# Kernel optimization log

Hardware: AMD Instinct MI355X
Metric: run time of the kernel (lower is better)

Reference implementation:

```python
import jax, jax.numpy as jnp
import numpy as np
from jax import lax

N_HEADS = 16
TOP_K = 2
N_EXPERTS = 8

def layer_norm(x, w, b, eps=1e-5):
    mu = jnp.mean(x, axis=-1, keepdims=True)
    var = jnp.mean(jnp.square(x - mu), axis=-1, keepdims=True)
    return (x - mu) * lax.rsqrt(var + eps) * w + b

def attention(x, w_qkv, b_qkv, w_o, b_o):
    B, T, D = x.shape
    dh = D // N_HEADS
    qkv = x @ w_qkv + b_qkv                       # [B,T,3D]
    q, k, v = jnp.split(qkv, 3, axis=-1)
    q = q.reshape(B, T, N_HEADS, dh)
    k = k.reshape(B, T, N_HEADS, dh)
    v = v.reshape(B, T, N_HEADS, dh)
    scores = jnp.einsum('bqhd,bkhd->bhqk', q, k) / jnp.sqrt(jnp.float32(dh)).astype(x.dtype)
    probs = jax.nn.softmax(scores, axis=-1)
    ctx = jnp.einsum('bhqk,bkhd->bqhd', probs, v).reshape(B, T, D)
    return ctx @ w_o + b_o

def moe_ff(x, w_gate, w1, b1, w2, b2):
    # top-k token routing (dropless: equivalent math to gate_and_sort ->
    # dispatch -> grouped expert GEMM -> combine -> unpermute)
    B, T, D = x.shape
    t = x.reshape(B * T, D)                        # [N,D]
    probs = jax.nn.softmax(t @ w_gate, axis=-1)    # [N,E]
    tw, ti = lax.top_k(probs, TOP_K)               # [N,K]
    tw = tw / jnp.sum(tw, axis=-1, keepdims=True)  # renormalize top-k weights
    out = jnp.zeros_like(t)
    for e in range(N_EXPERTS):
        we = jnp.sum(jnp.where(ti == e, tw, 0.0), axis=-1)       # [N]
        h = jax.nn.gelu(t @ w1[e] + b1[e]) @ w2[e] + b2[e]       # expert FFN
        out = out + we[:, None] * h
    return out.reshape(B, T, D)

def reference(x, ln1_w, ln1_b, ln2_w, ln2_b, w_qkv, b_qkv, w_o, b_o, w_gate, w1, b1, w2, b2):
    # pre-norm transformer block: attention then MoE FFN, both residual.
    # The torch module's 2-way micro-batch pipelining is per-token identical
    # to full-batch compute, so we compute the full batch at once.
    h = x + attention(layer_norm(x, ln1_w, ln1_b), w_qkv, b_qkv, w_o, b_o)
    return h + moe_ff(layer_norm(h, ln2_w, ln2_b), w_gate, w1, b1, w2, b2)

def setup_inputs() -> dict:
    key = jax.random.key(0)
    ks = jax.random.split(key, 8)
    B, T, D, H, E = 4, 512, 1024, 4096, 8
    s = lambda d: 1.0 / np.sqrt(d)
    return {
        'x': jax.random.normal(ks[0], (B, T, D), jnp.float32),
        'ln1_w': jnp.ones((D,), jnp.float32),
        'ln1_b': jnp.zeros((D,), jnp.float32),
        'ln2_w': jnp.ones((D,), jnp.float32),
        'ln2_b': jnp.zeros((D,), jnp.float32),
        'w_qkv': jax.random.normal(ks[1], (D, 3 * D), jnp.float32) * s(D),
        'b_qkv': jnp.zeros((3 * D,), jnp.float32),
        'w_o': jax.random.normal(ks[2], (D, D), jnp.float32) * s(D),
        'b_o': jnp.zeros((D,), jnp.float32),
        'w_gate': jax.random.normal(ks[3], (D, E), jnp.float32) * s(D),
        'w1': jax.random.normal(ks[4], (E, D, H), jnp.float32) * s(D),
        'b1': jnp.zeros((E, H), jnp.float32),
        'w2': jax.random.normal(ks[5], (E, H, D), jnp.float32) * s(H),
        'b2': jnp.zeros((E, D), jnp.float32),
    }
```

## Files before the change

### kernel.cpp

```cpp
#include <hip/hip_runtime.h>
#include <math.h>

typedef unsigned short ushort_t;
using short8 = __attribute__((ext_vector_type(8))) short;
using f32x4  = __attribute__((ext_vector_type(4))) float;

#define N_TOK 2048
#define DIM   1024
#define D3    3072
#define NHEAD 16
#define DH    64
#define TT    512
#define HID   4096
#define NEXP  8

__device__ __forceinline__ float bf2f(ushort_t u){
  union { unsigned int i; float f; } x; x.i = ((unsigned int)u) << 16; return x.f;
}
__device__ __forceinline__ ushort_t f2bf(float f){
  union { unsigned int i; float f; } x; x.f = f;
  unsigned int r = x.i + 0x7fffu + ((x.i >> 16) & 1u);
  return (ushort_t)(r >> 16);
}
__device__ __forceinline__ float gelu_f(float x){
  const float c = 0.7978845608028654f;
  float t = tanhf(c * (x + 0.044715f * x * x * x));
  return 0.5f * x * (1.0f + t);
}

template<int MODE>
__global__ __launch_bounds__(256) void ln_k(const float* __restrict__ xin,
                                            const float* __restrict__ w,
                                            const float* __restrict__ b,
                                            float* __restrict__ out,
                                            ushort_t* __restrict__ outhi,
                                            ushort_t* __restrict__ outlo){
  int tok = blockIdx.x;
  int t = threadIdx.x;
  float vals[4]; float s = 0.f, ss = 0.f;
#pragma unroll
  for (int i = 0; i < 4; i++){
    int d = t + i * 256;
    float v = xin[(size_t)tok * DIM + d];
    vals[i] = v; s += v; ss += v * v;
  }
  __shared__ float rs[256], rq[256];
  rs[t] = s; rq[t] = ss; __syncthreads();
  for (int k = 128; k > 0; k >>= 1){
    if (t < k){ rs[t] += rs[t + k]; rq[t] += rq[t + k]; }
    __syncthreads();
  }
  float mu  = rs[0] * (1.0f / DIM);
  float var = rq[0] * (1.0f / DIM) - mu * mu;
  float inv = rsqrtf(var + 1e-5f);
#pragma unroll
  for (int i = 0; i < 4; i++){
    int d = t + i * 256;
    float r = (vals[i] - mu) * inv * w[d] + b[d];
    size_t idx = (size_t)tok * DIM + d;
    if (MODE == 1){
      out[idx] = r;
      outhi[idx] = f2bf(r);
    } else {
      ushort_t hv = f2bf(r);
      outhi[idx] = hv;
      outlo[idx] = f2bf(r - bf2f(hv));
    }
  }
}

__global__ __launch_bounds__(256) void convT2(const float* __restrict__ src,
                                              ushort_t* __restrict__ dhi,
                                              ushort_t* __restrict__ dlo,
                                              int R, int C){
  __shared__ float tile[64][65];
  int r0 = blockIdx.y * 64, c0 = blockIdx.x * 64;
  int t = threadIdx.x;
  int tc = t & 15, tr = t >> 4;
#pragma unroll
  for (int i = 0; i < 4; i++){
    int r = tr + i * 16;
    float4 v = *(const float4*)&src[(size_t)(r0 + r) * C + c0 + tc * 4];
    tile[r][tc*4 + 0] = v.x; tile[r][tc*4 + 1] = v.y;
    tile[r][tc*4 + 2] = v.z; tile[r][tc*4 + 3] = v.w;
  }
  __syncthreads();
#pragma unroll
  for (int i = 0; i < 4; i++){
    int c = tr + i * 16;
    float v0 = tile[tc*4 + 0][c];
    float v1 = tile[tc*4 + 1][c];
    float v2 = tile[tc*4 + 2][c];
    float v3 = tile[tc*4 + 3][c];
    ushort4 oh, ol;
    oh.x = f2bf(v0); ol.x = f2bf(v0 - bf2f(oh.x));
    oh.y = f2bf(v1); ol.y = f2bf(v1 - bf2f(oh.y));
    oh.z = f2bf(v2); ol.z = f2bf(v2 - bf2f(oh.z));
    oh.w = f2bf(v3); ol.w = f2bf(v3 - bf2f(oh.w));
    size_t o = (size_t)(c0 + c) * R + r0 + tc * 4;
    *(ushort4*)&dhi[o] = oh;
    *(ushort4*)&dlo[o] = ol;
  }
}

__global__ __launch_bounds__(256) void convT_g(const float* __restrict__ src0,
                                               ushort_t* __restrict__ dst0,
                                               int R, int C){
  size_t eo = (size_t)blockIdx.z * R * C;
  const float* src = src0 + eo;
  ushort_t* dst = dst0 + eo;
  __shared__ float tile[64][65];
  int r0 = blockIdx.y * 64, c0 = blockIdx.x * 64;
  int t = threadIdx.x;
  int tc = t & 15, tr = t >> 4;
#pragma unroll
  for (int i = 0; i < 4; i++){
    int r = tr + i * 16;
    float4 v = *(const float4*)&src[(size_t)(r0 + r) * C + c0 + tc * 4];
    tile[r][tc*4 + 0] = v.x; tile[r][tc*4 + 1] = v.y;
    tile[r][tc*4 + 2] = v.z; tile[r][tc*4 + 3] = v.w;
  }
  __syncthreads();
#pragma unroll
  for (int i = 0; i < 4; i++){
    int c = tr + i * 16;
    ushort4 o;
    o.x = f2bf(tile[tc*4 + 0][c]);
    o.y = f2bf(tile[tc*4 + 1][c]);
    o.z = f2bf(tile[tc*4 + 2][c]);
    o.w = f2bf(tile[tc*4 + 3][c]);
    *(ushort4*)&dst[(size_t)(c0 + c) * R + r0 + tc * 4] = o;
  }
}

#define TBM 128
#define TBN 128
#define TBK 32
#define LDK 40

template<int EPI>
__global__ __launch_bounds__(256) void gemm_split(
    const ushort_t* __restrict__ Ahi, const ushort_t* __restrict__ Alo,
    const ushort_t* __restrict__ Bhi, const ushort_t* __restrict__ Blo,
    const float* __restrict__ bias,
    float* __restrict__ C, const float* __restrict__ Res,
    int Nn, int K)
{
  int bm = blockIdx.y * TBM, bn = blockIdx.x * TBN;
  __shared__ ushort_t Ah[TBM * LDK];
  __shared__ ushort_t Al[TBM * LDK];
  __shared__ ushort_t Bh[TBN * LDK];
  __shared__ ushort_t Bl[TBN * LDK];
  int t = threadIdx.x;
  int lane = t & 63, wave = t >> 6;
  int wm = (wave & 1) * 64, wn = (wave >> 1) * 64;

  int r0 = t >> 2, r1 = r0 + 64;
  int kc = (t & 3) * 8;
  const ushort_t* ah0 = Ahi + (size_t)(bm + r0) * K + kc;
  const ushort_t* ah1 = Ahi + (size_t)(bm + r1) * K + kc;
  const ushort_t* al0 = Alo + (size_t)(bm + r0) * K + kc;
  const ushort_t* al1 = Alo + (size_t)(bm + r1) * K + kc;
  const ushort_t* bh0 = Bhi + (size_t)(bn + r0) * K + kc;
  const ushort_t* bh1 = Bhi + (size_t)(bn + r1) * K + kc;
  const ushort_t* bl0 = Blo + (size_t)(bn + r0) * K + kc;
  const ushort_t* bl1 = Blo + (size_t)(bn + r1) * K + kc;

  f32x4 acc[4][4] = {};
  int fm = lane & 15, fk = (lane >> 4) * 8;

  for (int k0 = 0; k0 < K; k0 += TBK){
    uint4 vah0 = *(const uint4*)(ah0 + k0);
    uint4 vah1 = *(const uint4*)(ah1 + k0);
    uint4 val0 = *(const uint4*)(al0 + k0);
    uint4 val1 = *(const uint4*)(al1 + k0);
    uint4 vbh0 = *(const uint4*)(bh0 + k0);
    uint4 vbh1 = *(const uint4*)(bh1 + k0);
    uint4 vbl0 = *(const uint4*)(bl0 + k0);
    uint4 vbl1 = *(const uint4*)(bl1 + k0);
    *(uint4*)&Ah[r0 * LDK + kc] = vah0;
    *(uint4*)&Ah[r1 * LDK + kc] = vah1;
    *(uint4*)&Al[r0 * LDK + kc] = val0;
    *(uint4*)&Al[r1 * LDK + kc] = val1;
    *(uint4*)&Bh[r0 * LDK + kc] = vbh0;
    *(uint4*)&Bh[r1 * LDK + kc] = vbh1;
    *(uint4*)&Bl[r0 * LDK + kc] = vbl0;
    *(uint4*)&Bl[r1 * LDK + kc] = vbl1;
    __syncthreads();
    short8 afh[4], afl[4], bfh[4], bfl[4];
#pragma unroll
    for (int mi = 0; mi < 4; mi++){
      afh[mi] = *(const short8*)&Ah[(wm + mi*16 + fm) * LDK + fk];
      afl[mi] = *(const short8*)&Al[(wm + mi*16 + fm) * LDK + fk];
    }
#pragma unroll
    for (int nj = 0; nj < 4; nj++){
      bfh[nj] = *(const short8*)&Bh[(wn + nj*16 + fm) * LDK + fk];
      bfl[nj] = *(const short8*)&Bl[(wn + nj*16 + fm) * LDK + fk];
    }
#pragma unroll
    for (int mi = 0; mi < 4; mi++)
#pragma unroll
      for (int nj = 0; nj < 4; nj++){
        acc[mi][nj] = __builtin_amdgcn_mfma_f32_16x16x32_bf16(afh[mi], bfh[nj], acc[mi][nj], 0, 0, 0);
        acc[mi][nj] = __builtin_amdgcn_mfma_f32_16x16x32_bf16(afh[mi], bfl[nj], acc[mi][nj], 0, 0, 0);
        acc[mi][nj] = __builtin_amdgcn_mfma_f32_16x16x32_bf16(afl[mi], bfh[nj], acc[mi][nj], 0, 0, 0);
      }
    __syncthreads();
  }

#pragma unroll
  for (int mi = 0; mi < 4; mi++){
    int rowbase = bm + wm + mi*16 + (lane >> 4) * 4;
#pragma unroll
    for (int nj = 0; nj < 4; nj++){
      int n = bn + wn + nj*16 + (lane & 15);
      f32x4 v = acc[mi][nj];
#pragma unroll
      for (int rg = 0; rg < 4; rg++){
        size_t idx = (size_t)(rowbase + rg) * Nn + n;
        float val = v[rg] + bias[n];
        if (EPI == 1) val += Res[idx];
        C[idx] = val;
      }
    }
  }
}

__global__ __launch_bounds__(256) void scores_k(const float* __restrict__ qkv,
                                                float* __restrict__ S){
  int bh = blockIdx.z; int b = bh >> 4, h = bh & 15;
  int q0 = blockIdx.y * 64, k0 = blockIdx.x * 64;
  __shared__ float Qs[64][68];
  __shared__ float Ks[64][68];
  int t = threadIdx.x;
  int r = t >> 2, dp = (t & 3) * 16;
  {
    const float* qp = qkv + (size_t)(b * TT + q0 + r) * D3 + h * DH + dp;
    const float* kp = qkv + (size_t)(b * TT + k0 + r) * D3 + DIM + h * DH + dp;
#pragma unroll
    for (int c = 0; c < 4; c++){
      float4 qv = *(const float4*)(qp + c * 4);
      float4 kv = *(const float4*)(kp + c * 4);
      Qs[dp + c*4 + 0][r] = qv.x; Qs[dp + c*4 + 1][r] = qv.y;
      Qs[dp + c*4 + 2][r] = qv.z; Qs[dp + c*4 + 3][r] = qv.w;
      Ks[dp + c*4 + 0][r] = kv.x; Ks[dp + c*4 + 1][r] = kv.y;
      Ks[dp + c*4 + 2][r] = kv.z; Ks[dp + c*4 + 3][r] = kv.w;
    }
  }
  __syncthreads();
  int tx = t & 15, ty = t >> 4;
  float acc[4][4] = {};
#pragma unroll 8
  for (int d = 0; d < 64; d++){
    float4 qv = *(const float4*)&Qs[d][ty * 4];
    float4 kv = *(const float4*)&Ks[d][tx * 4];
    float qa[4] = {qv.x,qv.y,qv.z,qv.w};
    float ka[4] = {kv.x,kv.y,kv.z,kv.w};
#pragma unroll
    for (int i = 0; i < 4; i++)
#pragma unroll
      for (int j = 0; j < 4; j++)
        acc[i][j] += qa[i] * ka[j];
  }
#pragma unroll
  for (int i = 0; i < 4; i++)
#pragma unroll
    for (int j = 0; j < 4; j++)
      S[((size_t)bh * TT + q0 + ty*4 + i) * TT + k0 + tx*4 + j] = acc[i][j] * 0.125f;
}

__global__ __launch_bounds__(256) void softmax_k(float* __restrict__ S){
  size_t row = blockIdx.x;
  float* p = S + row * TT;
  int t = threadIdx.x;
  float v0 = p[t], v1 = p[t + 256];
  __shared__ float red[256];
  red[t] = fmaxf(v0, v1); __syncthreads();
  for (int k = 128; k > 0; k >>= 1){ if (t < k) red[t] = fmaxf(red[t], red[t + k]); __syncthreads(); }
  float m = red[0]; __syncthreads();
  float e0 = expf(v0 - m), e1 = expf(v1 - m);
  red[t] = e0 + e1; __syncthreads();
  for (int k = 128; k > 0; k >>= 1){ if (t < k) red[t] += red[t + k]; __syncthreads(); }
  float inv = 1.0f / red[0];
  p[t] = e0 * inv; p[t + 256] = e1 * inv;
}

__global__ __launch_bounds__(256) void ctx_k(const float* __restrict__ P,
                                             const float* __restrict__ qkv,
                                             ushort_t* __restrict__ chi,
                                             ushort_t* __restrict__ clo){
  int bh = blockIdx.y; int b = bh >> 4, h = bh & 15;
  int q0 = blockIdx.x * 64;
  __shared__ float Ps[16][68];
  __shared__ float Vs[16][68];
  int t = threadIdx.x;
  int tx = t & 15, ty = t >> 4;
  int pq = t >> 2, pk = (t & 3) * 4;
  int vk = t >> 4, vd = (t & 15) * 4;
  float acc[4][4] = {};
  for (int kk = 0; kk < TT; kk += 16){
    float4 pv = *(const float4*)&P[((size_t)bh * TT + q0 + pq) * TT + kk + pk];
    Ps[pk + 0][pq] = pv.x; Ps[pk + 1][pq] = pv.y;
    Ps[pk + 2][pq] = pv.z; Ps[pk + 3][pq] = pv.w;
    float4 vv = *(const float4*)&qkv[(size_t)(b * TT + kk + vk) * D3 + 2 * DIM + h * DH + vd];
    Vs[vk][vd + 0] = vv.x; Vs[vk][vd + 1] = vv.y;
    Vs[vk][vd + 2] = vv.z; Vs[vk][vd + 3] = vv.w;
    __syncthreads();
#pragma unroll
    for (int k = 0; k < 16; k++){
      float4 a = *(const float4*)&Ps[k][ty * 4];
      float4 bb = *(const float4*)&Vs[k][tx * 4];
      float aa[4] = {a.x,a.y,a.z,a.w};
      float bv[4] = {bb.x,bb.y,bb.z,bb.w};
#pragma unroll
      for (int i = 0; i < 4; i++)
#pragma unroll
        for (int j = 0; j < 4; j++)
          acc[i][j] += aa[i] * bv[j];
    }
    __syncthreads();
  }
#pragma unroll
  for (int i = 0; i < 4; i++)
#pragma unroll
    for (int j = 0; j < 4; j++){
      float v = acc[i][j];
      size_t idx = (size_t)(b * TT + q0 + ty*4 + i) * DIM + h * DH + tx*4 + j;
      ushort_t hv = f2bf(v);
      chi[idx] = hv;
      clo[idx] = f2bf(v - bf2f(hv));
    }
}

__global__ __launch_bounds__(256) void gate_k(const float* __restrict__ ln2f,
                                              const float* __restrict__ wg,
                                              float* __restrict__ we){
  int tok = blockIdx.x * 4 + (threadIdx.x >> 6);
  int lane = threadIdx.x & 63;
  float acc[8] = {};
  for (int d = lane; d < DIM; d += 64){
    float x = ln2f[(size_t)tok * DIM + d];
    float4 w0 = *(const float4*)&wg[d * 8];
    float4 w1v = *(const float4*)&wg[d * 8 + 4];
    float wv[8] = {w0.x,w0.y,w0.z,w0.w,w1v.x,w1v.y,w1v.z,w1v.w};
#pragma unroll
    for (int e = 0; e < 8; e++) acc[e] += x * wv[e];
  }
#pragma unroll
  for (int off = 32; off > 0; off >>= 1){
#pragma unroll
    for (int e = 0; e < 8; e++) acc[e] += __shfl_down(acc[e], off);
  }
  if (lane == 0){
    float m = acc[0];
    for (int e = 1; e < 8; e++) m = fmaxf(m, acc[e]);
    float pr[8], s = 0.f;
    for (int e = 0; e < 8; e++){ pr[e] = expf(acc[e] - m); s += pr[e]; }
    for (int e = 0; e < 8; e++) pr[e] /= s;
    int i0 = 0;
    for (int e = 1; e < 8; e++) if (pr[e] > pr[i0]) i0 = e;
    int i1 = (i0 == 0) ? 1 : 0;
    for (int e = 0; e < 8; e++) if (e != i0 && pr[e] > pr[i1]) i1 = e;
    float sm = pr[i0] + pr[i1];
    for (int e = 0; e < 8; e++)
      we[(size_t)tok * 8 + e] = (e == i0) ? pr[i0] / sm : ((e == i1) ? pr[i1] / sm : 0.f);
  }
}

__global__ __launch_bounds__(256) void route_k(const float* __restrict__ we,
                                               int* __restrict__ cnt,
                                               int* __restrict__ gidx,
                                               float* __restrict__ gw){
  int tok = blockIdx.x * 256 + threadIdx.x;
#pragma unroll
  for (int e = 0; e < NEXP; e++){
    float w = we[(size_t)tok * NEXP + e];
    if (w > 0.f){
      int p = atomicAdd(&cnt[e], 1);
      gidx[e * N_TOK + p] = tok;
      gw[e * N_TOK + p] = w;
    }
  }
}

__global__ void scan_k(const int* __restrict__ cnt, int* __restrict__ off){
  if (threadIdx.x == 0){
    int s = 0;
    for (int e = 0; e < NEXP; e++){ off[e] = s; s += cnt[e]; }
  }
}

template<int EPI>
__global__ __launch_bounds__(256) void moe_gemm_g(
    const ushort_t* __restrict__ A,
    const ushort_t* __restrict__ BT_all,
    const float* __restrict__ bias_all,
    ushort_t* __restrict__ Obf,
    float* __restrict__ Of,
    const int* __restrict__ gidx_all,
    const float* __restrict__ gw_all,
    const int* __restrict__ cnt,
    const int* __restrict__ off,
    int Nn, int K)
{
  int e  = blockIdx.y >> 4;
  int c  = cnt[e];
  int bm = (blockIdx.y & 15) * TBM;
  if (bm >= c) return;
  int bn = blockIdx.x * TBN;
  const int* gidx = gidx_all + e * N_TOK;
  const float* gwp = gw_all + e * N_TOK;
  const ushort_t* BT = BT_all + (size_t)e * Nn * K;
  const float* bias = bias_all + (size_t)e * Nn;
  int obase = off[e];

  __shared__ ushort_t As[TBM * LDK];
  __shared__ ushort_t Bs[TBN * LDK];
  int t = threadIdx.x;
  int lane = t & 63, wave = t >> 6;
  int wm = (wave & 1) * 64, wn = (wave >> 1) * 64;

  int r0 = t >> 2, r1 = r0 + 64;
  int kc = (t & 3) * 8;
  size_t ga0, ga1;
  if (EPI == 0){
    int g0 = bm + r0, g1 = bm + r1;
    ga0 = (size_t)((g0 < c) ? gidx[g0] : gidx[bm]);
    ga1 = (size_t)((g1 < c) ? gidx[g1] : gidx[bm]);
  } else {
    int mx = 2 * N_TOK - 1;
    int g0 = obase + bm + r0; if (g0 > mx) g0 = mx;
    int g1 = obase + bm + r1; if (g1 > mx) g1 = mx;
    ga0 = (size_t)g0; ga1 = (size_t)g1;
  }
  const ushort_t* a0p = A + ga0 * K + kc;
  const ushort_t* a1p = A + ga1 * K + kc;
  const ushort_t* b0p = BT + (size_t)(bn + r0) * K + kc;
  const ushort_t* b1p = BT + (size_t)(bn + r1) * K + kc;

  f32x4 acc[4][4] = {};
  int fm = lane & 15, fk = (lane >> 4) * 8;

  uint4 av0 = *(const uint4*)(a0p);
  uint4 av1 = *(const uint4*)(a1p);
  uint4 bv0 = *(const uint4*)(b0p);
  uint4 bv1 = *(const uint4*)(b1p);

  for (int k0 = 0; k0 < K; k0 += TBK){
    *(uint4*)&As[r0 * LDK + kc] = av0;
    *(uint4*)&As[r1 * LDK + kc] = av1;
    *(uint4*)&Bs[r0 * LDK + kc] = bv0;
    *(uint4*)&Bs[r1 * LDK + kc] = bv1;
    __syncthreads();
    int kn = k0 + TBK;
    if (kn < K){
      av0 = *(const uint4*)(a0p + kn);
      av1 = *(const uint4*)(a1p + kn);
      bv0 = *(const uint4*)(b0p + kn);
      bv1 = *(const uint4*)(b1p + kn);
    }
    short8 af[4], bfr[4];
#pragma unroll
    for (int mi = 0; mi < 4; mi++)
      af[mi] = *(const short8*)&As[(wm + mi*16 + fm) * LDK + fk];
#pragma unroll
    for (int nj = 0; nj < 4; nj++)
      bfr[nj] = *(const short8*)&Bs[(wn + nj*16 + fm) * LDK + fk];
#pragma unroll
    for (int mi = 0; mi < 4; mi++)
#pragma unroll
      for (int nj = 0; nj < 4; nj++)
        acc[mi][nj] = __builtin_amdgcn_mfma_f32_16x16x32_bf16(af[mi], bfr[nj], acc[mi][nj], 0, 0, 0);
    __syncthreads();
  }

#pragma unroll
  for (int mi = 0; mi < 4; mi++){
    int rowbase = bm + wm + mi*16 + (lane >> 4) * 4;
#pragma unroll
    for (int nj = 0; nj < 4; nj++){
      int n = bn + wn + nj*16 + (lane & 15);
      f32x4 v = acc[mi][nj];
#pragma unroll
      for (int rg = 0; rg < 4; rg++){
        int r = rowbase + rg;
        if (r < c){
          float val = v[rg] + bias[n];
          if (EPI == 0){
            Obf[(size_t)(obase + r) * Nn + n] = f2bf(gelu_f(val));
          } else {
            int tok = gidx[r];
            atomicAdd(&Of[(size_t)tok * Nn + n], gwp[r] * val);
          }
        }
      }
    }
  }
}

__global__ __launch_bounds__(256) void final_k(const float* __restrict__ h,
                                               const float* __restrict__ acc,
                                               float* __restrict__ out){
  size_t i = (size_t)blockIdx.x * 256 + threadIdx.x;
  out[i] = h[i] + acc[i];
}

extern "C" void kernel_launch(void* const* d_in, const int* in_sizes, int n_in,
                              void* d_out, int out_size, void* d_ws, size_t ws_size,
                              hipStream_t stream){
  const float* x     = (const float*)d_in[0];
  const float* ln1w  = (const float*)d_in[1];
  const float* ln1b  = (const float*)d_in[2];
  const float* ln2w  = (const float*)d_in[3];
  const float* ln2b  = (const float*)d_in[4];
  const float* wqkv  = (const float*)d_in[5];
  const float* bqkv  = (const float*)d_in[6];
  const float* wo    = (const float*)d_in[7];
  const float* bo    = (const float*)d_in[8];
  const float* wgate = (const float*)d_in[9];
  const float* w1    = (const float*)d_in[10];
  const float* b1    = (const float*)d_in[11];
  const float* w2    = (const float*)d_in[12];
  const float* b2    = (const float*)d_in[13];

  char* ws = (char*)d_ws;
  const size_t MB = 1024 * 1024;
  float*    hbuf  = (float*)(ws + 0 * MB);
  ushort_t* ln1hi = (ushort_t*)(ws + 0 * MB);
  ushort_t* ln1lo = (ushort_t*)(ws + 4 * MB);
  float*    accb  = (float*)(ws + 8 * MB);
  ushort_t* wqkvThi = (ushort_t*)(ws + 8 * MB);
  ushort_t* wqkvTlo = (ushort_t*)(ws + 14 * MB);
  ushort_t* ln2bf = (ushort_t*)(ws + 16 * MB);
  ushort_t* h1e   = (ushort_t*)(ws + 20 * MB);
  float*    qkv   = (float*)(ws + 20 * MB);
  float*    ln2f  = (float*)(ws + 24 * MB);
  ushort_t* ctxhi = (ushort_t*)(ws + 44 * MB);
  ushort_t* ctxlo = (ushort_t*)(ws + 48 * MB);
  ushort_t* woThi = (ushort_t*)(ws + 52 * MB);
  ushort_t* woTlo = (ushort_t*)(ws + 54 * MB);
  float*    sc    = (float*)(ws + 56 * MB);
  ushort_t* wTe   = (ushort_t*)(ws + 56 * MB);
  float*    webuf = (float*)(ws + 120 * MB);
  int*      cnt   = (int*)  (ws + 120 * MB + 256 * 1024);
  int*      off   = (int*)  (ws + 120 * MB + 260 * 1024);
  int*      bidx  = (int*)  (ws + 120 * MB + 320 * 1024);
  float*    bw    = (float*)(ws + 120 * MB + 448 * 1024);

  ln_k<2><<<N_TOK, 256, 0, stream>>>(x, ln1w, ln1b, nullptr, ln1hi, ln1lo);
  convT2<<<dim3(D3 / 64, DIM / 64), 256, 0, stream>>>(wqkv, wqkvThi, wqkvTlo, DIM, D3);
  gemm_split<0><<<dim3(D3 / TBN, N_TOK / TBM), 256, 0, stream>>>(
      ln1hi, ln1lo, wqkvThi, wqkvTlo, bqkv, qkv, nullptr, D3, DIM);
  scores_k<<<dim3(8, 8, 64), 256, 0, stream>>>(qkv, sc);
  softmax_k<<<64 * TT, 256, 0, stream>>>(sc);
  ctx_k<<<dim3(8, 64), 256, 0, stream>>>(sc, qkv, ctxhi, ctxlo);
  convT_g<<<dim3(HID / 64, DIM / 64, NEXP), 256, 0, stream>>>(w1, wTe, DIM, HID);
  convT2<<<dim3(DIM / 64, DIM / 64), 256, 0, stream>>>(wo, woThi, woTlo, DIM, DIM);
  gemm_split<1><<<dim3(DIM / TBN, N_TOK / TBM), 256, 0, stream>>>(
      ctxhi, ctxlo, woThi, woTlo, bo, hbuf, x, DIM, DIM);
  ln_k<1><<<N_TOK, 256, 0, stream>>>(hbuf, ln2w, ln2b, ln2f, ln2bf, nullptr);
  gate_k<<<N_TOK / 4, 256, 0, stream>>>(ln2f, wgate, webuf);

  hipMemsetAsync(cnt, 0, 32, stream);
  hipMemsetAsync(accb, 0, (size_t)N_TOK * DIM * 4, stream);
  route_k<<<N_TOK / 256, 256, 0, stream>>>(webuf, cnt, bidx, bw);
  scan_k<<<1, 64, 0, stream>>>(cnt, off);
  moe_gemm_g<0><<<dim3(HID / TBN, NEXP * 16), 256, 0, stream>>>(
      ln2bf, wTe, b1, h1e, nullptr, bidx, bw, cnt, off, HID, DIM);
  convT_g<<<dim3(DIM / 64, HID / 64, NEXP), 256, 0, stream>>>(w2, wTe, HID, DIM);
  moe_gemm_g<1><<<dim3(DIM / TBN, NEXP * 16), 256, 0, stream>>>(
      h1e, wTe, b2, nullptr, accb, bidx, bw, cnt, off, DIM, HID);
  final_k<<<(N_TOK * DIM) / 256, 256, 0, stream>>>(hbuf, accb, (float*)d_out);
}
```

Before: 772.9 us.

## Split-K the second MoE GEMM, remap block indices, prefetch in split GEMM

The second expert GEMM (K=4096) is split into four K-chunks of 1024, multiplying its block count. The chunks combine through the existing atomicAdd epilogue, with bias added only by the first chunk. The MoE kernels now use a 1D grid that interleaves experts across consecutive block IDs, and their K loop is unrolled by two with double register prefetch. The split-precision GEMMs get a remapped block order meant to help L2 locality/XCD spread, plus register prefetch of the next K tile. The cost is four times more atomic traffic into the accumulator and more register pressure.

```diff
diff --git a/kernel.cpp b/kernel.cpp
--- a/kernel.cpp
+++ b/kernel.cpp
@@ -144,9 +144,12 @@
     const ushort_t* __restrict__ Bhi, const ushort_t* __restrict__ Blo,
     const float* __restrict__ bias,
     float* __restrict__ C, const float* __restrict__ Res,
-    int Nn, int K)
+    int Nn, int K, int mblocks)
 {
-  int bm = blockIdx.y * TBM, bn = blockIdx.x * TBN;
+  int q = gridDim.x >> 3;
+  int L = (blockIdx.x & 7) * q + (blockIdx.x >> 3);
+  int bm = (L % mblocks) * TBM;
+  int bn = (L / mblocks) * TBN;
   __shared__ ushort_t Ah[TBM * LDK];
   __shared__ ushort_t Al[TBM * LDK];
   __shared__ ushort_t Bh[TBN * LDK];
@@ -169,15 +172,16 @@
   f32x4 acc[4][4] = {};
   int fm = lane & 15, fk = (lane >> 4) * 8;
 
+  uint4 vah0 = *(const uint4*)(ah0);
+  uint4 vah1 = *(const uint4*)(ah1);
+  uint4 val0 = *(const uint4*)(al0);
+  uint4 val1 = *(const uint4*)(al1);
+  uint4 vbh0 = *(const uint4*)(bh0);
+  uint4 vbh1 = *(const uint4*)(bh1);
+  uint4 vbl0 = *(const uint4*)(bl0);
+  uint4 vbl1 = *(const uint4*)(bl1);
+
   for (int k0 = 0; k0 < K; k0 += TBK){
-    uint4 vah0 = *(const uint4*)(ah0 + k0);
-    uint4 vah1 = *(const uint4*)(ah1 + k0);
-    uint4 val0 = *(const uint4*)(al0 + k0);
-    uint4 val1 = *(const uint4*)(al1 + k0);
-    uint4 vbh0 = *(const uint4*)(bh0 + k0);
-    uint4 vbh1 = *(const uint4*)(bh1 + k0);
-    uint4 vbl0 = *(const uint4*)(bl0 + k0);
-    uint4 vbl1 = *(const uint4*)(bl1 + k0);
     *(uint4*)&Ah[r0 * LDK + kc] = vah0;
     *(uint4*)&Ah[r1 * LDK + kc] = vah1;
     *(uint4*)&Al[r0 * LDK + kc] = val0;
@@ -187,6 +191,17 @@
     *(uint4*)&Bl[r0 * LDK + kc] = vbl0;
     *(uint4*)&Bl[r1 * LDK + kc] = vbl1;
     __syncthreads();
+    int kn = k0 + TBK;
+    if (kn < K){
+      vah0 = *(const uint4*)(ah0 + kn);
+      vah1 = *(const uint4*)(ah1 + kn);
+      val0 = *(const uint4*)(al0 + kn);
+      val1 = *(const uint4*)(al1 + kn);
+      vbh0 = *(const uint4*)(bh0 + kn);
+      vbh1 = *(const uint4*)(bh1 + kn);
+      vbl0 = *(const uint4*)(bl0 + kn);
+      vbl1 = *(const uint4*)(bl1 + kn);
+    }
     short8 afh[4], afl[4], bfh[4], bfl[4];
 #pragma unroll
     for (int mi = 0; mi < 4; mi++){
@@ -402,13 +417,20 @@
     const float* __restrict__ gw_all,
     const int* __restrict__ cnt,
     const int* __restrict__ off,
-    int Nn, int K)
+    int Nn)
 {
-  int e  = blockIdx.y >> 4;
-  int c  = cnt[e];
-  int bm = (blockIdx.y & 15) * TBM;
+  int rid = blockIdx.x;
+  int e = rid & 7;
+  int s = rid >> 3;
+  int c = cnt[e];
+  int bm = (s & 15) * TBM;
   if (bm >= c) return;
-  int bn = blockIdx.x * TBN;
+  int col, ks;
+  if (EPI == 0){ col = s >> 4; ks = 0; }
+  else         { col = (s >> 4) & 7; ks = s >> 7; }
+  const int K = (EPI == 0) ? DIM : HID;
+  int kbase = ks * 1024;
+  int bn = col * TBN;
   const int* gidx = gidx_all + e * N_TOK;
   const float* gwp = gw_all + e * N_TOK;
   const ushort_t* BT = BT_all + (size_t)e * Nn * K;
@@ -434,44 +456,78 @@
     int g1 = obase + bm + r1; if (g1 > mx) g1 = mx;
     ga0 = (size_t)g0; ga1 = (size_t)g1;
   }
-  const ushort_t* a0p = A + ga0 * K + kc;
-  const ushort_t* a1p = A + ga1 * K + kc;
-  const ushort_t* b0p = BT + (size_t)(bn + r0) * K + kc;
-  const ushort_t* b1p = BT + (size_t)(bn + r1) * K + kc;
+  const ushort_t* a0p = A + ga0 * K + kbase + kc;
+  const ushort_t* a1p = A + ga1 * K + kbase + kc;
+  const ushort_t* b0p = BT + (size_t)(bn + r0) * K + kbase + kc;
+  const ushort_t* b1p = BT + (size_t)(bn + r1) * K + kbase + kc;
 
   f32x4 acc[4][4] = {};
   int fm = lane & 15, fk = (lane >> 4) * 8;
 
-  uint4 av0 = *(const uint4*)(a0p);
-  uint4 av1 = *(const uint4*)(a1p);
-  uint4 bv0 = *(const uint4*)(b0p);
-  uint4 bv1 = *(const uint4*)(b1p);
-
-  for (int k0 = 0; k0 < K; k0 += TBK){
-    *(uint4*)&As[r0 * LDK + kc] = av0;
-    *(uint4*)&As[r1 * LDK + kc] = av1;
-    *(uint4*)&Bs[r0 * LDK + kc] = bv0;
-    *(uint4*)&Bs[r1 * LDK + kc] = bv1;
-    __syncthreads();
-    int kn = k0 + TBK;
-    if (kn < K){
-      av0 = *(const uint4*)(a0p + kn);
-      av1 = *(const uint4*)(a1p + kn);
-      bv0 = *(const uint4*)(b0p + kn);
-      bv1 = *(const uint4*)(b1p + kn);
-    }
-    short8 af[4], bfr[4];
-#pragma unroll
-    for (int mi = 0; mi < 4; mi++)
-      af[mi] = *(const short8*)&As[(wm + mi*16 + fm) * LDK + fk];
-#pragma unroll
-    for (int nj = 0; nj < 4; nj++)
-      bfr[nj] = *(const short8*)&Bs[(wn + nj*16 + fm) * LDK + fk];
-#pragma unroll
-    for (int mi = 0; mi < 4; mi++)
+  uint4 Aa0 = *(const uint4*)(a0p);
+  uint4 Aa1 = *(const uint4*)(a1p);
+  uint4 Ba0 = *(const uint4*)(b0p);
+  uint4 Ba1 = *(const uint4*)(b1p);
+  uint4 Ab0 = *(const uint4*)(a0p + TBK);
+  uint4 Ab1 = *(const uint4*)(a1p + TBK);
+  uint4 Bb0 = *(const uint4*)(b0p + TBK);
+  uint4 Bb1 = *(const uint4*)(b1p + TBK);
+
+  const int KSTEPS = 32;
+  for (int it = 0; it < KSTEPS; it += 2){
+    *(uint4*)&As[r0 * LDK + kc] = Aa0;
+    *(uint4*)&As[r1 * LDK + kc] = Aa1;
+    *(uint4*)&Bs[r0 * LDK + kc] = Ba0;
+    *(uint4*)&Bs[r1 * LDK + kc] = Ba1;
+    __syncthreads();
+    if (it + 2 < KSTEPS){
+      int kn = (it + 2) * TBK;
+      Aa0 = *(const uint4*)(a0p + kn);
+      Aa1 = *(const uint4*)(a1p + kn);
+      Ba0 = *(const uint4*)(b0p + kn);
+      Ba1 = *(const uint4*)(b1p + kn);
+    }
+    {
+      short8 af[4], bfr[4];
+#pragma unroll
+      for (int mi = 0; mi < 4; mi++)
+        af[mi] = *(const short8*)&As[(wm + mi*16 + fm) * LDK + fk];
 #pragma unroll
       for (int nj = 0; nj < 4; nj++)
-        acc[mi][nj] = __builtin_amdgcn_mfma_f32_16x16x32_bf16(af[mi], bfr[nj], acc[mi][nj], 0, 0, 0);
+        bfr[nj] = *(const short8*)&Bs[(wn + nj*16 + fm) * LDK + fk];
+#pragma unroll
+      for (int mi = 0; mi < 4; mi++)
+#pragma unroll
+        for (int nj = 0; nj < 4; nj++)
+          acc[mi][nj] = __builtin_amdgcn_mfma_f32_16x16x32_bf16(af[mi], bfr[nj], acc[mi][nj], 0, 0, 0);
+    }
+    __syncthreads();
+    *(uint4*)&As[r0 * LDK + kc] = Ab0;
+    *(uint4*)&As[r1 * LDK + kc] = Ab1;
+    *(uint4*)&Bs[r0 * LDK + kc] = Bb0;
+    *(uint4*)&Bs[r1 * LDK + kc] = Bb1;
+    __syncthreads();
+    if (it + 3 < KSTEPS){
+      int kn = (it + 3) * TBK;
+      Ab0 = *(const uint4*)(a0p + kn);
+      Ab1 = *(const uint4*)(a1p + kn);
+      Bb0 = *(const uint4*)(b0p + kn);
+      Bb1 = *(const uint4*)(b1p + kn);
+    }
+    {
+      short8 af[4], bfr[4];
+#pragma unroll
+      for (int mi = 0; mi < 4; mi++)
+        af[mi] = *(const short8*)&As[(wm + mi*16 + fm) * LDK + fk];
+#pragma unroll
+      for (int nj = 0; nj < 4; nj++)
+        bfr[nj] = *(const short8*)&Bs[(wn + nj*16 + fm) * LDK + fk];
+#pragma unroll
+      for (int mi = 0; mi < 4; mi++)
+#pragma unroll
+        for (int nj = 0; nj < 4; nj++)
+          acc[mi][nj] = __builtin_amdgcn_mfma_f32_16x16x32_bf16(af[mi], bfr[nj], acc[mi][nj], 0, 0, 0);
+    }
     __syncthreads();
   }
 
@@ -486,10 +542,12 @@
       for (int rg = 0; rg < 4; rg++){
         int r = rowbase + rg;
         if (r < c){
-          float val = v[rg] + bias[n];
           if (EPI == 0){
+            float val = v[rg] + bias[n];
             Obf[(size_t)(obase + r) * Nn + n] = f2bf(gelu_f(val));
           } else {
+            float val = v[rg];
+            if (ks == 0) val += bias[n];
             int tok = gidx[r];
             atomicAdd(&Of[(size_t)tok * Nn + n], gwp[r] * val);
           }
@@ -550,15 +608,15 @@
 
   ln_k<2><<<N_TOK, 256, 0, stream>>>(x, ln1w, ln1b, nullptr, ln1hi, ln1lo);
   convT2<<<dim3(D3 / 64, DIM / 64), 256, 0, stream>>>(wqkv, wqkvThi, wqkvTlo, DIM, D3);
-  gemm_split<0><<<dim3(D3 / TBN, N_TOK / TBM), 256, 0, stream>>>(
-      ln1hi, ln1lo, wqkvThi, wqkvTlo, bqkv, qkv, nullptr, D3, DIM);
+  gemm_split<0><<<(N_TOK / TBM) * (D3 / TBN), 256, 0, stream>>>(
+      ln1hi, ln1lo, wqkvThi, wqkvTlo, bqkv, qkv, nullptr, D3, DIM, N_TOK / TBM);
   scores_k<<<dim3(8, 8, 64), 256, 0, stream>>>(qkv, sc);
   softmax_k<<<64 * TT, 256, 0, stream>>>(sc);
   ctx_k<<<dim3(8, 64), 256, 0, stream>>>(sc, qkv, ctxhi, ctxlo);
   convT_g<<<dim3(HID / 64, DIM / 64, NEXP), 256, 0, stream>>>(w1, wTe, DIM, HID);
   convT2<<<dim3(DIM / 64, DIM / 64), 256, 0, stream>>>(wo, woThi, woTlo, DIM, DIM);
-  gemm_split<1><<<dim3(DIM / TBN, N_TOK / TBM), 256, 0, stream>>>(
-      ctxhi, ctxlo, woThi, woTlo, bo, hbuf, x, DIM, DIM);
+  gemm_split<1><<<(N_TOK / TBM) * (DIM / TBN), 256, 0, stream>>>(
+      ctxhi, ctxlo, woThi, woTlo, bo, hbuf, x, DIM, DIM, N_TOK / TBM);
   ln_k<1><<<N_TOK, 256, 0, stream>>>(hbuf, ln2w, ln2b, ln2f, ln2bf, nullptr);
   gate_k<<<N_TOK / 4, 256, 0, stream>>>(ln2f, wgate, webuf);
 
@@ -566,10 +624,10 @@
   hipMemsetAsync(accb, 0, (size_t)N_TOK * DIM * 4, stream);
   route_k<<<N_TOK / 256, 256, 0, stream>>>(webuf, cnt, bidx, bw);
   scan_k<<<1, 64, 0, stream>>>(cnt, off);
-  moe_gemm_g<0><<<dim3(HID / TBN, NEXP * 16), 256, 0, stream>>>(
-      ln2bf, wTe, b1, h1e, nullptr, bidx, bw, cnt, off, HID, DIM);
+  moe_gemm_g<0><<<NEXP * 16 * (HID / TBN), 256, 0, stream>>>(
+      ln2bf, wTe, b1, h1e, nullptr, bidx, bw, cnt, off, HID);
   convT_g<<<dim3(DIM / 64, HID / 64, NEXP), 256, 0, stream>>>(w2, wTe, HID, DIM);
-  moe_gemm_g<1><<<dim3(DIM / TBN, NEXP * 16), 256, 0, stream>>>(
-      h1e, wTe, b2, nullptr, accb, bidx, bw, cnt, off, DIM, HID);
+  moe_gemm_g<1><<<NEXP * 16 * (DIM / TBN) * 4, 256, 0, stream>>>(
+      h1e, wTe, b2, nullptr, accb, bidx, bw, cnt, off, DIM);
   final_k<<<(N_TOK * DIM) / 256, 256, 0, stream>>>(hbuf, accb, (float*)d_out);
 }
```

Result: slower. 882.4 us (+14.2%).
